# Optimization experiments

Measured on AMD Instinct MI355X. Metric: run time of the kernel, lower is better.

Reference implementation:

```python
import jax, jax.numpy as jnp
import numpy as np

B, N, S, K = 8, 16384, 1024, 32
C_STEM, C_PATCH, PE_DIM = 64, 128, 24
RADIUS = 0.2
NUM_BANDS = PE_DIM // 6  # 4 freq bands, sin+cos per xyz axis -> 3*2*4 = 24


def setup_inputs() -> dict:
    key = jax.random.key(0)
    ks = jax.random.split(key, 6)
    xyz = jax.random.uniform(ks[0], (B, N, 3), dtype=jnp.float32)
    point_feature = jax.random.normal(ks[1], (B, N, C_STEM), dtype=jnp.float32)
    patch_center = jax.random.uniform(ks[2], (B, S, 3), dtype=jnp.float32)
    in_dim = C_STEM + 3 + PE_DIM  # grouped_feature + relative_xyz + pos-enc
    w1 = jax.random.normal(ks[3], (in_dim, C_PATCH), dtype=jnp.float32) / np.sqrt(in_dim)
    b1 = jnp.zeros((C_PATCH,), dtype=jnp.float32)
    w2 = jax.random.normal(ks[4], (C_PATCH, C_PATCH), dtype=jnp.float32) / np.sqrt(C_PATCH)
    b2 = jnp.zeros((C_PATCH,), dtype=jnp.float32)
    return dict(xyz=xyz, point_feature=point_feature, patch_center=patch_center,
                w1=w1, b1=b1, w2=w2, b2=b2)


def query_ball_point(radius, nsample, xyz, new_xyz):
    # Standard PointNet++ ball query. xyz:[B,N,3], new_xyz:[B,S,3] -> idx:[B,S,K]
    n = xyz.shape[1]
    sqrdists = jnp.sum((new_xyz[:, :, None, :] - xyz[:, None, :, :]) ** 2, axis=-1)  # [B,S,N]
    gi = jnp.where(sqrdists > radius * radius, n,
                   jnp.arange(n, dtype=jnp.int32)[None, None, :])
    gi = jnp.sort(gi, axis=-1)[:, :, :nsample]           # first K in-ball indices
    first = gi[:, :, :1]
    gi = jnp.where(gi == n, first, gi)                   # pad misses with first hit
    return jnp.minimum(gi, n - 1)


def index_points(points, idx):
    # points:[B,N,C], idx:[B,S,K] -> [B,S,K,C]
    b = points.shape[0]
    return points[jnp.arange(b)[:, None, None], idx]


def pos_encode(rel):
    # NeRF-style sinusoidal encoding of relative xyz: [...,3] -> [...,PE_DIM]
    freqs = (2.0 ** jnp.arange(NUM_BANDS, dtype=jnp.float32)) * jnp.pi
    ang = rel[..., None] * freqs                          # [...,3,NB]
    enc = jnp.concatenate([jnp.sin(ang), jnp.cos(ang)], axis=-1)  # [...,3,2NB]
    return enc.reshape(rel.shape[:-1] + (PE_DIM,))


def reference(xyz, point_feature, patch_center, w1, b1, w2, b2):
    neighbor_idx = query_ball_point(RADIUS, K, xyz, patch_center)   # [B,S,K]
    grouped_xyz = index_points(xyz, neighbor_idx)                    # [B,S,K,3]
    grouped_feature = index_points(point_feature, neighbor_idx)      # [B,S,K,C_STEM]
    relative_xyz = grouped_xyz - patch_center[:, :, None, :]
    relative_position = pos_encode(relative_xyz)                     # [B,S,K,PE_DIM]
    grouped_input = jnp.concatenate(
        (grouped_feature, relative_xyz, relative_position), axis=-1)  # [B,S,K,91]
    h = jax.nn.relu(grouped_input @ w1 + b1)   # PointMLP 1 (shared per-point MLP)
    h = h @ w2 + b2                            # PointMLP 2 (no activation)
    patch_feature = jnp.max(h, axis=2)         # max-pool over K neighbors -> [B,S,C_PATCH]
    return (patch_feature, neighbor_idx)
```

## Files before the change

### kernel.cpp

```cpp
#include <hip/hip_runtime.h>
#include <hip/hip_bf16.h>

#define B_ 8
#define N_ 16384
#define S_ 1024
#define K_ 32
#define CSTEM 64
#define CPATCH 128
#define INDIM 91
#define LDA 104
#define LDH 136
#define NQ 2

typedef __attribute__((ext_vector_type(8))) short short8v;
typedef __attribute__((ext_vector_type(4))) float f32x4;

static __device__ __forceinline__ unsigned short f2bf(float f) {
  union { float f; unsigned int u; } v; v.f = f;
  return (unsigned short)((v.u + 0x7FFFu + ((v.u >> 16) & 1u)) >> 16);
}

__global__ __launch_bounds__(256) void pack_weights(
    const float* __restrict__ w1, const float* __restrict__ w2,
    unsigned short* __restrict__ w1p, unsigned short* __restrict__ w2p)
{
  const int id = blockIdx.x * 256 + threadIdx.x;
  if (id < 3 * 8 * 64) {
    const int l = id & 63, ct = (id >> 6) & 7, ks = id >> 9;
    const int col = 16 * ct + (l & 15);
    const int kb = 32 * ks + (l >> 4) * 8;
    unsigned short v[8];
    #pragma unroll
    for (int j = 0; j < 8; ++j) {
      const int k = kb + j;
      v[j] = (k < INDIM) ? f2bf(w1[k * CPATCH + col]) : (unsigned short)0;
    }
    *(short8v*)&w1p[(size_t)id * 8] = *(const short8v*)v;
  } else if (id < 3 * 8 * 64 + 4 * 8 * 64) {
    const int id2 = id - 3 * 8 * 64;
    const int l = id2 & 63, ct = (id2 >> 6) & 7, ks = id2 >> 9;
    const int col = 16 * ct + (l & 15);
    const int kb = 32 * ks + (l >> 4) * 8;
    unsigned short v[8];
    #pragma unroll
    for (int j = 0; j < 8; ++j) v[j] = f2bf(w2[(kb + j) * CPATCH + col]);
    *(short8v*)&w2p[(size_t)id2 * 8] = *(const short8v*)v;
  }
}

#define FCOMP(V, IDX) (((IDX) & 3) == 0 ? (V)[(IDX) >> 2].x : \
                       ((IDX) & 3) == 1 ? (V)[(IDX) >> 2].y : \
                       ((IDX) & 3) == 2 ? (V)[(IDX) >> 2].z : (V)[(IDX) >> 2].w)

__global__ __launch_bounds__(256) void ball_query_kernel(
    const float* __restrict__ xyz, const float* __restrict__ pc,
    float* __restrict__ idx_out)
{
  const int lane = threadIdx.x & 63;
  const int w    = threadIdx.x >> 6;
  const int bs   = blockIdx.x * 4 + w;
  const int b    = bs >> 10;

  __shared__ int sidx[4][K_];

  const float* __restrict__ xb = xyz + (size_t)b * N_ * 3;
  const float cx = pc[bs * 3 + 0];
  const float cy = pc[bs * 3 + 1];
  const float cz = pc[bs * 3 + 2];
  const double rr = 0.2 * 0.2;

  int found = 0;
  for (int base = 0; base < N_; base += 1024) {
    const int i0 = base + lane * 16;
    float4 v[12];
    #pragma unroll
    for (int t = 0; t < 12; ++t)
      v[t] = *(const float4*)&xb[i0 * 3 + t * 4];

    unsigned mask = 0u;
    #pragma unroll
    for (int p = 0; p < 16; ++p) {
      const float X = FCOMP(v, 3 * p + 0);
      const float Y = FCOMP(v, 3 * p + 1);
      const float Z = FCOMP(v, 3 * p + 2);
      const float dxf = X - cx, dyf = Y - cy, dzf = Z - cz;
      const float d2f = fmaf(dxf, dxf, fmaf(dyf, dyf, dzf * dzf));
      bool in;
      if (fabsf(d2f - 0.04f) <= 1e-5f) {
        const double dx = (double)X - (double)cx;
        const double dy = (double)Y - (double)cy;
        const double dz = (double)Z - (double)cz;
        in = (dx * dx + dy * dy + dz * dz) <= rr;
      } else {
        in = (d2f < 0.04f);
      }
      if (in) mask |= (1u << p);
    }

    const int cnt = __popc(mask);
    int incl = cnt;
    #pragma unroll
    for (int d = 1; d < 64; d <<= 1) {
      const int t = __shfl_up(incl, d);
      if (lane >= d) incl += t;
    }
    const int tot = __shfl(incl, 63);

    int pos = found + (incl - cnt);
    #pragma unroll
    for (int p = 0; p < 16; ++p) {
      if (mask & (1u << p)) {
        if (pos < K_) sidx[w][pos] = i0 + p;
        ++pos;
      }
    }
    found += tot;
    if (found >= K_) break;
  }

  if (lane == 0 && found == 0) sidx[w][0] = N_ - 1;
  __threadfence_block();
  if (lane < K_) {
    const int fill = sidx[w][0];
    const int v = (lane < found) ? sidx[w][lane] : fill;
    idx_out[(size_t)bs * K_ + lane] = (float)v;
  }
}

__global__ __launch_bounds__(256) void patch_mlp_mfma(
    const float* __restrict__ xyz, const float* __restrict__ pf,
    const float* __restrict__ pc,
    const unsigned short* __restrict__ w1p, const float* __restrict__ b1,
    const unsigned short* __restrict__ w2p, const float* __restrict__ b2,
    const float* __restrict__ idx_f, float* __restrict__ out)
{
  const int tid  = threadIdx.x;
  const int lane = tid & 63;
  const int w    = tid >> 6;
  const int bs0  = blockIdx.x * NQ;
  const int b    = bs0 >> 10;

  __shared__ float scen[3 * NQ];
  __shared__ int   sidx[NQ][K_];
  __shared__ __align__(16) unsigned short As[NQ * K_][LDA];
  __shared__ __align__(16) unsigned short Hs[K_][LDH];

  const float* __restrict__ xb  = xyz + (size_t)b * N_ * 3;
  const float* __restrict__ pfb = pf  + (size_t)b * N_ * CSTEM;

  if (tid < 3 * NQ) scen[tid] = pc[bs0 * 3 + tid];
  if (tid < NQ * K_) {
    const int q = tid >> 5, j = tid & 31;
    sidx[q][j] = (int)idx_f[(size_t)(bs0 + q) * K_ + j];
  }
  __syncthreads();

  short8v w1f[3][2], w2f[4][2];
  #pragma unroll
  for (int ks = 0; ks < 3; ++ks)
    #pragma unroll
    for (int t = 0; t < 2; ++t)
      w1f[ks][t] = *(const short8v*)&w1p[((size_t)(ks * 8 + 2 * w + t) * 64 + lane) * 8];
  #pragma unroll
  for (int ks = 0; ks < 4; ++ks)
    #pragma unroll
    for (int t = 0; t < 2; ++t)
      w2f[ks][t] = *(const short8v*)&w2p[((size_t)(ks * 8 + 2 * w + t) * 64 + lane) * 8];
  const float bias1[2] = { b1[32 * w + (lane & 15)], b1[32 * w + 16 + (lane & 15)] };
  const float bias2[2] = { b2[32 * w + (lane & 15)], b2[32 * w + 16 + (lane & 15)] };

  {
    const int row = tid >> 3, sub = tid & 7;
    #pragma unroll
    for (int q = 0; q < NQ; ++q) {
      const int r = sidx[q][row];
      const float4 f0 = *(const float4*)&pfb[(size_t)r * CSTEM + sub * 8];
      const float4 f1 = *(const float4*)&pfb[(size_t)r * CSTEM + sub * 8 + 4];
      unsigned short vv[8];
      vv[0] = f2bf(f0.x); vv[1] = f2bf(f0.y); vv[2] = f2bf(f0.z); vv[3] = f2bf(f0.w);
      vv[4] = f2bf(f1.x); vv[5] = f2bf(f1.y); vv[6] = f2bf(f1.z); vv[7] = f2bf(f1.w);
      *(short8v*)&As[q * K_ + row][sub * 8] = *(const short8v*)vv;
    }
  }
  {
    const int row = tid & 31, j = tid >> 5;
    #pragma unroll
    for (int q = 0; q < NQ; ++q) {
      const int r = sidx[q][row];
      const float r0 = xb[r * 3 + 0] - scen[q * 3 + 0];
      const float r1 = xb[r * 3 + 1] - scen[q * 3 + 1];
      const float r2 = xb[r * 3 + 2] - scen[q * 3 + 2];
      #pragma unroll
      for (int cc = 0; cc < 4; ++cc) {
        const int c = 64 + 4 * j + cc;
        float val;
        if (c < 67) val = (c == 64) ? r0 : ((c == 65) ? r1 : r2);
        else if (c < 91) {
          const int qq = c - 67, d = qq >> 3, rbit = qq & 7, band = rbit & 3;
          const float rel = (d == 0) ? r0 : ((d == 1) ? r1 : r2);
          const float ang = rel * ((float)(1 << band) * 3.14159265358979323846f);
          val = (rbit < 4) ? __sinf(ang) : __cosf(ang);
        } else val = 0.f;
        As[q * K_ + row][c] = f2bf(val);
      }
    }
  }
  __syncthreads();

  #pragma unroll 1
  for (int q = 0; q < NQ; ++q) {
    f32x4 acc[2][2] = {};
    #pragma unroll
    for (int ks = 0; ks < 3; ++ks) {
      const int k0 = ks * 32 + (lane >> 4) * 8;
      const short8v a0 = *(const short8v*)&As[q * K_ + (lane & 15)][k0];
      const short8v a1 = *(const short8v*)&As[q * K_ + 16 + (lane & 15)][k0];
      acc[0][0] = __builtin_amdgcn_mfma_f32_16x16x32_bf16(a0, w1f[ks][0], acc[0][0], 0, 0, 0);
      acc[0][1] = __builtin_amdgcn_mfma_f32_16x16x32_bf16(a0, w1f[ks][1], acc[0][1], 0, 0, 0);
      acc[1][0] = __builtin_amdgcn_mfma_f32_16x16x32_bf16(a1, w1f[ks][0], acc[1][0], 0, 0, 0);
      acc[1][1] = __builtin_amdgcn_mfma_f32_16x16x32_bf16(a1, w1f[ks][1], acc[1][1], 0, 0, 0);
    }
    #pragma unroll
    for (int rt = 0; rt < 2; ++rt)
      #pragma unroll
      for (int t = 0; t < 2; ++t)
        #pragma unroll
        for (int reg = 0; reg < 4; ++reg) {
          const float h = fmaxf(acc[rt][t][reg] + bias1[t], 0.f);
          const int row = 16 * rt + (lane >> 4) * 4 + reg;
          const int col = 32 * w + 16 * t + (lane & 15);
          Hs[row][col] = f2bf(h);
        }
    __syncthreads();

    f32x4 acc2[2][2] = {};
    #pragma unroll
    for (int ks = 0; ks < 4; ++ks) {
      const int k0 = ks * 32 + (lane >> 4) * 8;
      const short8v a0 = *(const short8v*)&Hs[(lane & 15)][k0];
      const short8v a1 = *(const short8v*)&Hs[16 + (lane & 15)][k0];
      acc2[0][0] = __builtin_amdgcn_mfma_f32_16x16x32_bf16(a0, w2f[ks][0], acc2[0][0], 0, 0, 0);
      acc2[0][1] = __builtin_amdgcn_mfma_f32_16x16x32_bf16(a0, w2f[ks][1], acc2[0][1], 0, 0, 0);
      acc2[1][0] = __builtin_amdgcn_mfma_f32_16x16x32_bf16(a1, w2f[ks][0], acc2[1][0], 0, 0, 0);
      acc2[1][1] = __builtin_amdgcn_mfma_f32_16x16x32_bf16(a1, w2f[ks][1], acc2[1][1], 0, 0, 0);
    }
    float m0 = -3.4e38f, m1 = -3.4e38f;
    #pragma unroll
    for (int rt = 0; rt < 2; ++rt)
      #pragma unroll
      for (int reg = 0; reg < 4; ++reg) {
        m0 = fmaxf(m0, acc2[rt][0][reg]);
        m1 = fmaxf(m1, acc2[rt][1][reg]);
      }
    m0 += bias2[0];
    m1 += bias2[1];
    m0 = fmaxf(m0, __shfl_xor(m0, 16));
    m0 = fmaxf(m0, __shfl_xor(m0, 32));
    m1 = fmaxf(m1, __shfl_xor(m1, 16));
    m1 = fmaxf(m1, __shfl_xor(m1, 32));
    if (lane < 16) {
      out[(size_t)(bs0 + q) * CPATCH + 32 * w + lane]      = m0;
      out[(size_t)(bs0 + q) * CPATCH + 32 * w + 16 + lane] = m1;
    }
    __syncthreads();
  }
}

extern "C" void kernel_launch(void* const* d_in, const int* in_sizes, int n_in,
                              void* d_out, int out_size, void* d_ws, size_t ws_size,
                              hipStream_t stream) {
  const float* xyz = (const float*)d_in[0];
  const float* pf  = (const float*)d_in[1];
  const float* pc  = (const float*)d_in[2];
  const float* w1  = (const float*)d_in[3];
  const float* b1  = (const float*)d_in[4];
  const float* w2  = (const float*)d_in[5];
  const float* b2  = (const float*)d_in[6];

  float* out     = (float*)d_out;
  float* idx_out = out + (size_t)B_ * S_ * CPATCH;

  unsigned short* w1p = (unsigned short*)d_ws;
  unsigned short* w2p = w1p + 96 * 128;

  pack_weights<<<14, 256, 0, stream>>>(w1, w2, w1p, w2p);
  ball_query_kernel<<<B_ * S_ / 4, 256, 0, stream>>>(xyz, pc, idx_out);
  patch_mlp_mfma<<<B_ * S_ / NQ, 256, 0, stream>>>(xyz, pf, pc, w1p, b1, w2p, b2,
                                                   idx_out, out);
}
```

Before: 53.79 us.

## Move neighbor gather and positional encoding into ball-query kernel as MFMA fragments

The ball query kernel now gathers the neighbor features and computes the relative xyz and sinusoidal encoding itself. It writes them to a workspace buffer as bf16, already arranged in MFMA A-fragment order. The MLP kernel then loads these fragments straight into registers, with no shared-memory A staging, no index reload and no extra barrier, and it handles 4 patches per block instead of 2. The aim is to remove the separate gather phase and LDS traffic from the MLP kernel. The cost is an extra global write and read of about 50 MB of intermediate bf16 data.

```diff
diff --git a/kernel.cpp b/kernel.cpp
--- a/kernel.cpp
+++ b/kernel.cpp
@@ -8,9 +8,9 @@
 #define CSTEM 64
 #define CPATCH 128
 #define INDIM 91
-#define LDA 104
 #define LDH 136
-#define NQ 2
+#define NQ 4
+#define AFRAG 3072
 
 typedef __attribute__((ext_vector_type(8))) short short8v;
 typedef __attribute__((ext_vector_type(4))) float f32x4;
@@ -18,6 +18,36 @@
 static __device__ __forceinline__ unsigned short f2bf(float f) {
   union { float f; unsigned int u; } v; v.f = f;
   return (unsigned short)((v.u + 0x7FFFu + ((v.u >> 16) & 1u)) >> 16);
+}
+
+static __device__ __forceinline__ short8v cvt8(const float4 a, const float4 b) {
+  unsigned short v[8];
+  v[0] = f2bf(a.x); v[1] = f2bf(a.y); v[2] = f2bf(a.z); v[3] = f2bf(a.w);
+  v[4] = f2bf(b.x); v[5] = f2bf(b.y); v[6] = f2bf(b.z); v[7] = f2bf(b.w);
+  return *(const short8v*)v;
+}
+
+static __device__ __forceinline__ short8v pe_frag(
+    float r0, float r1, float r2, int kq)
+{
+  unsigned short v[8];
+  #pragma unroll
+  for (int j = 0; j < 8; ++j) {
+    const int c = 64 + kq + j;
+    float val;
+    if (c < 67) {
+      val = (c == 64) ? r0 : ((c == 65) ? r1 : r2);
+    } else if (c < 91) {
+      const int qq = c - 67, d = qq >> 3, rbit = qq & 7, band = rbit & 3;
+      const float rel = (d == 0) ? r0 : ((d == 1) ? r1 : r2);
+      const float ang = rel * ((float)(1 << band) * 3.14159265358979323846f);
+      val = (rbit < 4) ? __sinf(ang) : __cosf(ang);
+    } else {
+      val = 0.f;
+    }
+    v[j] = f2bf(val);
+  }
+  return *(const short8v*)v;
 }
 
 __global__ __launch_bounds__(256) void pack_weights(
@@ -52,18 +82,21 @@
                        ((IDX) & 3) == 1 ? (V)[(IDX) >> 2].y : \
                        ((IDX) & 3) == 2 ? (V)[(IDX) >> 2].z : (V)[(IDX) >> 2].w)
 
-__global__ __launch_bounds__(256) void ball_query_kernel(
-    const float* __restrict__ xyz, const float* __restrict__ pc,
-    float* __restrict__ idx_out)
+__global__ __launch_bounds__(256) void ball_gather_kernel(
+    const float* __restrict__ xyz, const float* __restrict__ pf,
+    const float* __restrict__ pc,
+    unsigned short* __restrict__ agather, float* __restrict__ idx_out)
 {
   const int lane = threadIdx.x & 63;
   const int w    = threadIdx.x >> 6;
   const int bs   = blockIdx.x * 4 + w;
   const int b    = bs >> 10;
 
-  __shared__ int sidx[4][K_];
-
-  const float* __restrict__ xb = xyz + (size_t)b * N_ * 3;
+  __shared__ int   sidx[4][K_];
+  __shared__ float sxyz[4][K_][3];
+
+  const float* __restrict__ xb  = xyz + (size_t)b * N_ * 3;
+  const float* __restrict__ pfb = pf  + (size_t)b * N_ * CSTEM;
   const float cx = pc[bs * 3 + 0];
   const float cy = pc[bs * 3 + 1];
   const float cz = pc[bs * 3 + 2];
@@ -110,7 +143,12 @@
     #pragma unroll
     for (int p = 0; p < 16; ++p) {
       if (mask & (1u << p)) {
-        if (pos < K_) sidx[w][pos] = i0 + p;
+        if (pos < K_) {
+          sidx[w][pos] = i0 + p;
+          sxyz[w][pos][0] = FCOMP(v, 3 * p + 0);
+          sxyz[w][pos][1] = FCOMP(v, 3 * p + 1);
+          sxyz[w][pos][2] = FCOMP(v, 3 * p + 2);
+        }
         ++pos;
       }
     }
@@ -118,42 +156,61 @@
     if (found >= K_) break;
   }
 
-  if (lane == 0 && found == 0) sidx[w][0] = N_ - 1;
+  if (lane == 0 && found == 0) {
+    sidx[w][0] = N_ - 1;
+    sxyz[w][0][0] = xb[(N_ - 1) * 3 + 0];
+    sxyz[w][0][1] = xb[(N_ - 1) * 3 + 1];
+    sxyz[w][0][2] = xb[(N_ - 1) * 3 + 2];
+  }
   __threadfence_block();
+
   if (lane < K_) {
-    const int fill = sidx[w][0];
+    const int   fill = sidx[w][0];
+    const float fx = sxyz[w][0][0];
+    const float fy = sxyz[w][0][1];
+    const float fz = sxyz[w][0][2];
     const int v = (lane < found) ? sidx[w][lane] : fill;
+    if (lane >= found) {
+      sidx[w][lane] = fill;
+      sxyz[w][lane][0] = fx;
+      sxyz[w][lane][1] = fy;
+      sxyz[w][lane][2] = fz;
+    }
     idx_out[(size_t)bs * K_ + lane] = (float)v;
   }
+  __threadfence_block();
+
+  unsigned short* __restrict__ ag = agather + (size_t)bs * AFRAG;
+  const int koff = (lane >> 4) * 8;
+  #pragma unroll
+  for (int rt = 0; rt < 2; ++rt) {
+    const int row = rt * 16 + (lane & 15);
+    const int r = sidx[w][row];
+    const float4 f0 = *(const float4*)&pfb[(size_t)r * CSTEM + koff];
+    const float4 f1 = *(const float4*)&pfb[(size_t)r * CSTEM + koff + 4];
+    const float4 g0 = *(const float4*)&pfb[(size_t)r * CSTEM + 32 + koff];
+    const float4 g1 = *(const float4*)&pfb[(size_t)r * CSTEM + 32 + koff + 4];
+    const float r0 = sxyz[w][row][0] - cx;
+    const float r1 = sxyz[w][row][1] - cy;
+    const float r2 = sxyz[w][row][2] - cz;
+    *(short8v*)&ag[((0 * 2 + rt) * 64 + lane) * 8] = cvt8(f0, f1);
+    *(short8v*)&ag[((1 * 2 + rt) * 64 + lane) * 8] = cvt8(g0, g1);
+    *(short8v*)&ag[((2 * 2 + rt) * 64 + lane) * 8] = pe_frag(r0, r1, r2, koff);
+  }
 }
 
 __global__ __launch_bounds__(256) void patch_mlp_mfma(
-    const float* __restrict__ xyz, const float* __restrict__ pf,
-    const float* __restrict__ pc,
+    const unsigned short* __restrict__ agather,
     const unsigned short* __restrict__ w1p, const float* __restrict__ b1,
     const unsigned short* __restrict__ w2p, const float* __restrict__ b2,
-    const float* __restrict__ idx_f, float* __restrict__ out)
+    float* __restrict__ out)
 {
   const int tid  = threadIdx.x;
   const int lane = tid & 63;
   const int w    = tid >> 6;
   const int bs0  = blockIdx.x * NQ;
-  const int b    = bs0 >> 10;
-
-  __shared__ float scen[3 * NQ];
-  __shared__ int   sidx[NQ][K_];
-  __shared__ __align__(16) unsigned short As[NQ * K_][LDA];
+
   __shared__ __align__(16) unsigned short Hs[K_][LDH];
-
-  const float* __restrict__ xb  = xyz + (size_t)b * N_ * 3;
-  const float* __restrict__ pfb = pf  + (size_t)b * N_ * CSTEM;
-
-  if (tid < 3 * NQ) scen[tid] = pc[bs0 * 3 + tid];
-  if (tid < NQ * K_) {
-    const int q = tid >> 5, j = tid & 31;
-    sidx[q][j] = (int)idx_f[(size_t)(bs0 + q) * K_ + j];
-  }
-  __syncthreads();
 
   short8v w1f[3][2], w2f[4][2];
   #pragma unroll
@@ -169,56 +226,21 @@
   const float bias1[2] = { b1[32 * w + (lane & 15)], b1[32 * w + 16 + (lane & 15)] };
   const float bias2[2] = { b2[32 * w + (lane & 15)], b2[32 * w + 16 + (lane & 15)] };
 
-  {
-    const int row = tid >> 3, sub = tid & 7;
-    #pragma unroll
-    for (int q = 0; q < NQ; ++q) {
-      const int r = sidx[q][row];
-      const float4 f0 = *(const float4*)&pfb[(size_t)r * CSTEM + sub * 8];
-      const float4 f1 = *(const float4*)&pfb[(size_t)r * CSTEM + sub * 8 + 4];
-      unsigned short vv[8];
-      vv[0] = f2bf(f0.x); vv[1] = f2bf(f0.y); vv[2] = f2bf(f0.z); vv[3] = f2bf(f0.w);
-      vv[4] = f2bf(f1.x); vv[5] = f2bf(f1.y); vv[6] = f2bf(f1.z); vv[7] = f2bf(f1.w);
-      *(short8v*)&As[q * K_ + row][sub * 8] = *(const short8v*)vv;
-    }
-  }
-  {
-    const int row = tid & 31, j = tid >> 5;
-    #pragma unroll
-    for (int q = 0; q < NQ; ++q) {
-      const int r = sidx[q][row];
-      const float r0 = xb[r * 3 + 0] - scen[q * 3 + 0];
-      const float r1 = xb[r * 3 + 1] - scen[q * 3 + 1];
-      const float r2 = xb[r * 3 + 2] - scen[q * 3 + 2];
-      #pragma unroll
-      for (int cc = 0; cc < 4; ++cc) {
-        const int c = 64 + 4 * j + cc;
-        float val;
-        if (c < 67) val = (c == 64) ? r0 : ((c == 65) ? r1 : r2);
-        else if (c < 91) {
-          const int qq = c - 67, d = qq >> 3, rbit = qq & 7, band = rbit & 3;
-          const float rel = (d == 0) ? r0 : ((d == 1) ? r1 : r2);
-          const float ang = rel * ((float)(1 << band) * 3.14159265358979323846f);
-          val = (rbit < 4) ? __sinf(ang) : __cosf(ang);
-        } else val = 0.f;
-        As[q * K_ + row][c] = f2bf(val);
-      }
-    }
-  }
-  __syncthreads();
-
-  #pragma unroll 1
+  #pragma unroll
   for (int q = 0; q < NQ; ++q) {
+    const unsigned short* __restrict__ ap = agather + (size_t)(bs0 + q) * AFRAG;
+    short8v af[6];
+    #pragma unroll
+    for (int f = 0; f < 6; ++f)
+      af[f] = *(const short8v*)&ap[((size_t)(f * 64) + lane) * 8];
+
     f32x4 acc[2][2] = {};
     #pragma unroll
     for (int ks = 0; ks < 3; ++ks) {
-      const int k0 = ks * 32 + (lane >> 4) * 8;
-      const short8v a0 = *(const short8v*)&As[q * K_ + (lane & 15)][k0];
-      const short8v a1 = *(const short8v*)&As[q * K_ + 16 + (lane & 15)][k0];
-      acc[0][0] = __builtin_amdgcn_mfma_f32_16x16x32_bf16(a0, w1f[ks][0], acc[0][0], 0, 0, 0);
-      acc[0][1] = __builtin_amdgcn_mfma_f32_16x16x32_bf16(a0, w1f[ks][1], acc[0][1], 0, 0, 0);
-      acc[1][0] = __builtin_amdgcn_mfma_f32_16x16x32_bf16(a1, w1f[ks][0], acc[1][0], 0, 0, 0);
-      acc[1][1] = __builtin_amdgcn_mfma_f32_16x16x32_bf16(a1, w1f[ks][1], acc[1][1], 0, 0, 0);
+      acc[0][0] = __builtin_amdgcn_mfma_f32_16x16x32_bf16(af[ks * 2 + 0], w1f[ks][0], acc[0][0], 0, 0, 0);
+      acc[0][1] = __builtin_amdgcn_mfma_f32_16x16x32_bf16(af[ks * 2 + 0], w1f[ks][1], acc[0][1], 0, 0, 0);
+      acc[1][0] = __builtin_amdgcn_mfma_f32_16x16x32_bf16(af[ks * 2 + 1], w1f[ks][0], acc[1][0], 0, 0, 0);
+      acc[1][1] = __builtin_amdgcn_mfma_f32_16x16x32_bf16(af[ks * 2 + 1], w1f[ks][1], acc[1][1], 0, 0, 0);
     }
     #pragma unroll
     for (int rt = 0; rt < 2; ++rt)
@@ -282,9 +304,9 @@
 
   unsigned short* w1p = (unsigned short*)d_ws;
   unsigned short* w2p = w1p + 96 * 128;
+  unsigned short* agather = w2p + 128 * 128;
 
   pack_weights<<<14, 256, 0, stream>>>(w1, w2, w1p, w2p);
-  ball_query_kernel<<<B_ * S_ / 4, 256, 0, stream>>>(xyz, pc, idx_out);
-  patch_mlp_mfma<<<B_ * S_ / NQ, 256, 0, stream>>>(xyz, pf, pc, w1p, b1, w2p, b2,
-                                                   idx_out, out);
-}
+  ball_gather_kernel<<<B_ * S_ / 4, 256, 0, stream>>>(xyz, pf, pc, agather, idx_out);
+  patch_mlp_mfma<<<B_ * S_ / NQ, 256, 0, stream>>>(agather, w1p, b1, w2p, b2, out);
+}
```

Result: slower. 60.63 us (+12.7%).
